# Kernel tuning notes

Measured on AMD Instinct MI355X. Metric: run time of the kernel, lower is better.

Reference implementation:

```python
import jax, jax.numpy as jnp
from jax import lax
import numpy as np

B, S, V, C, H, Z, NSTEP = 256, 128, 128, 16, 1024, 256, 128
VC = V * C


def _gru_cell(x, h, Wih, Whh, bih, bhh):
    # torch GRUCell: gates ordered r, z, n along rows of (3H, in)
    gi = x @ Wih.T + bih
    gh = h @ Whh.T + bhh
    ir, iz, inn = jnp.split(gi, 3, axis=-1)
    hr, hz, hn = jnp.split(gh, 3, axis=-1)
    r = jax.nn.sigmoid(ir + hr)
    zg = jax.nn.sigmoid(iz + hz)
    n = jnp.tanh(inn + r * hn)
    return (1.0 - zg) * n + zg * h


def setup_inputs() -> dict:
    key = jax.random.key(0)
    ks = jax.random.split(key, 32)
    sc = 0.05
    p = lambda k, shape: (jax.random.normal(k, shape, jnp.float32) * sc)
    inp = {
        "x": jax.random.normal(ks[0], (B, V, S), jnp.float32),
        "noise": jax.random.normal(ks[1], (B, Z), jnp.float32),
        "gruf_Wih": p(ks[2], (3 * H, V)), "gruf_Whh": p(ks[3], (3 * H, H)),
        "gruf_bih": p(ks[4], (3 * H,)), "gruf_bhh": p(ks[5], (3 * H,)),
        "grub_Wih": p(ks[6], (3 * H, V)), "grub_Whh": p(ks[7], (3 * H, H)),
        "grub_bih": p(ks[8], (3 * H,)), "grub_bhh": p(ks[9], (3 * H,)),
        "Wmu": p(ks[10], (Z, 2 * H)), "bmu": p(ks[11], (Z,)),
        "Wvar": p(ks[12], (Z, 2 * H)), "bvar": p(ks[13], (Z,)),
        "Winit": p(ks[14], (H, Z)), "binit": p(ks[15], (H,)),
        "c1_Wih": p(ks[16], (3 * H, Z + VC)), "c1_Whh": p(ks[17], (3 * H, H)),
        "c1_bih": p(ks[18], (3 * H,)), "c1_bhh": p(ks[19], (3 * H,)),
        "c2_Wih": p(ks[20], (3 * H, H)), "c2_Whh": p(ks[21], (3 * H, H)),
        "c2_bih": p(ks[22], (3 * H,)), "c2_bhh": p(ks[23], (3 * H,)),
        "Wout": p(ks[24], (VC, H)), "bout": p(ks[25], (VC,)),
    }
    return inp


def reference(x, noise, gruf_Wih, gruf_Whh, gruf_bih, gruf_bhh,
              grub_Wih, grub_Whh, grub_bih, grub_bhh,
              Wmu, bmu, Wvar, bvar, Winit, binit,
              c1_Wih, c1_Whh, c1_bih, c1_bhh,
              c2_Wih, c2_Whh, c2_bih, c2_bhh, Wout, bout):
    b = x.shape[0]
    xe = jnp.transpose(x, (0, 2, 1))           # (b, s, V)
    xt = jnp.swapaxes(xe, 0, 1)                # (s, b, V) time-major
    h0 = jnp.zeros((b, H), x.dtype)

    def step_f(h, xs):
        h2 = _gru_cell(xs, h, gruf_Wih, gruf_Whh, gruf_bih, gruf_bhh)
        return h2, None

    def step_b(h, xs):
        h2 = _gru_cell(xs, h, grub_Wih, grub_Whh, grub_bih, grub_bhh)
        return h2, None

    hf, _ = lax.scan(step_f, h0, xt)
    hb, _ = lax.scan(step_b, h0, xt[::-1])
    enc = jnp.concatenate([hf, hb], axis=-1)   # (b, 2H) = h_n transposed+flattened

    mu = enc @ Wmu.T + bmu
    var = jnp.exp(enc @ Wvar.T + bvar)         # Normal(mu, var): var is the scale
    z = mu + var * noise                       # rsample

    out0 = jnp.zeros((b, VC), x.dtype).at[:, -1].set(1.0)
    h1_0 = jnp.tanh(z @ Winit.T + binit)
    h2_0 = jnp.zeros((b, H), x.dtype)

    def dstep(carry, i):
        out, h1, h2 = carry
        inp = jnp.concatenate([out, z], axis=1)          # (b, VC + Z)
        h1n = _gru_cell(inp, h1, c1_Wih, c1_Whh, c1_bih, c1_bhh)
        h2_prev = jnp.where(i == 0, h1n, h2)             # hx[1] = hx[0] at step 0
        h2n = _gru_cell(h1n, h2_prev, c2_Wih, c2_Whh, c2_bih, c2_bhh)
        logits = h2n @ Wout.T + bout                     # (b, VC)
        ls = jax.nn.log_softmax(logits.reshape(b, C, V), axis=1).reshape(b, VC)
        # eval-mode _sampling: argmax -> one-hot (no gradient flows through it)
        out_n = jax.nn.one_hot(jnp.argmax(ls, axis=1), VC, dtype=ls.dtype)
        return (out_n, h1n, h2n), ls

    _, xs = lax.scan(dstep, (out0, h1_0, h2_0), jnp.arange(NSTEP))
    recon_seq = jnp.swapaxes(xs, 0, 1)                   # (b, n_step, VC)
    recon = jnp.transpose(recon_seq, (0, 2, 1)).reshape(b, C, V, NSTEP)
    return mu, var, z, recon
```

## Files before the change

kernel.cpp:

```cpp
#include <hip/hip_runtime.h>
#include <cstdint>
#include <cstddef>

typedef __attribute__((ext_vector_type(8))) short bf16x8;
typedef __attribute__((ext_vector_type(4))) float f32x4;
#define DEVI __device__ __forceinline__

constexpr int B = 256, S = 128, V = 128, C = 16, H = 1024, Z = 256, NSTEP = 128;
constexpr int VC = V * C, G3 = 3 * H;
constexpr size_t BVC = (size_t)B * VC;

typedef __attribute__((address_space(1))) const unsigned short* gas_p;
typedef __attribute__((address_space(3))) unsigned short* las_p;

DEVI unsigned short f2bf(float f){unsigned u=__float_as_uint(f);u+=0x7fffu+((u>>16)&1u);return (unsigned short)(u>>16);}
DEVI float sigm(float x){return 1.f/(1.f+expf(-x));}
DEVI f32x4 MFMA(bf16x8 a,bf16x8 b,f32x4 c){return __builtin_amdgcn_mfma_f32_16x16x32_bf16(a,b,c,0,0,0);}
DEVI void stage16(const unsigned short* g, unsigned short* l){__builtin_amdgcn_global_load_lds((gas_p)g,(las_p)l,16,0,0);}

DEVI unsigned long long ldc8(const void* p){return __hip_atomic_load((const unsigned long long*)p,__ATOMIC_RELAXED,__HIP_MEMORY_SCOPE_AGENT);}
DEVI void stc8(void* p, unsigned long long v){__hip_atomic_store((unsigned long long*)p,v,__ATOMIC_RELAXED,__HIP_MEMORY_SCOPE_AGENT);}
DEVI unsigned ldc4(const void* p){return __hip_atomic_load((const unsigned*)p,__ATOMIC_RELAXED,__HIP_MEMORY_SCOPE_AGENT);}
DEVI void stc4(void* p, unsigned v){__hip_atomic_store((unsigned*)p,v,__ATOMIC_RELAXED,__HIP_MEMORY_SCOPE_AGENT);}
DEVI unsigned long long pack4(float a,float b,float c,float d){
  return (unsigned long long)f2bf(a)|((unsigned long long)f2bf(b)<<16)|((unsigned long long)f2bf(c)<<32)|((unsigned long long)f2bf(d)<<48);
}
DEVI unsigned long long packf2(float a,float b){
  return (unsigned long long)__float_as_uint(a)|((unsigned long long)__float_as_uint(b)<<32);
}

DEVI void wv(int n){
  if(n==0)      asm volatile("s_waitcnt vmcnt(0)":::"memory");
  else if(n==2) asm volatile("s_waitcnt vmcnt(2)":::"memory");
  else if(n==3) asm volatile("s_waitcnt vmcnt(3)":::"memory");
  else if(n==4) asm volatile("s_waitcnt vmcnt(4)":::"memory");
  else if(n==6) asm volatile("s_waitcnt vmcnt(6)":::"memory");
}
DEVI void lg0(){asm volatile("s_waitcnt lgkmcnt(0)":::"memory");}
DEVI void cmb(){asm volatile("" ::: "memory");}

DEVI void waitflags(const unsigned* f,int base,int n,unsigned tgt){
  int lane=threadIdx.x&63;
  if (lane<n){
    const unsigned* a=&f[(size_t)(base+lane)<<4];
    while (ldc4(a)<tgt) __builtin_amdgcn_s_sleep(1);
  }
}
DEVI unsigned waitseq(const unsigned* f,int base,int n,unsigned tgt){
  int lane=threadIdx.x&63; unsigned v=tgt<<24;
  if (lane<n){
    const unsigned* a=&f[(size_t)(base+lane)<<4];
    v=ldc4(a);
    while ((v>>24)<tgt){__builtin_amdgcn_s_sleep(1); v=ldc4(a);}
  }
  return v;
}

__global__ void k_cvt(const float* __restrict__ src, unsigned short* __restrict__ dst, int n){
  for (int i=blockIdx.x*256+threadIdx.x;i<n;i+=gridDim.x*256) dst[i]=f2bf(src[i]);
}

__global__ void k_xt(const float* __restrict__ x, unsigned short* __restrict__ xtb){
  __shared__ float tile[32][33];
  int sb=blockIdx.x*32, rb=blockIdx.y*32, tx=threadIdx.x, ty=threadIdx.y;
  for (int i=ty;i<32;i+=8) tile[i][tx]=x[(size_t)(rb+i)*S+sb+tx];
  __syncthreads();
  for (int i=ty;i<32;i+=8) xtb[(size_t)(sb+i)*(B*V)+rb+tx]=f2bf(tile[tx][i]);
}

__global__ void k_wt(const float* __restrict__ w, float* __restrict__ wt){
  __shared__ float tile[32][33];
  int vb=blockIdx.x*32, nb=blockIdx.y*32, tx=threadIdx.x, ty=threadIdx.y;
  for (int i=ty;i<32;i+=8) tile[i][tx]=w[(size_t)(nb+i)*(VC+Z)+vb+tx];
  __syncthreads();
  for (int i=ty;i<32;i+=8) wt[(size_t)(vb+i)*G3+nb+tx]=tile[tx][i];
}

__global__ __launch_bounds__(256) void k_mu_var_z(const float* __restrict__ hf,const float* __restrict__ hb,
    const float* __restrict__ Wmu,const float* __restrict__ bmu,
    const float* __restrict__ Wvar,const float* __restrict__ bvar,
    const float* __restrict__ noise,
    float* __restrict__ omu,float* __restrict__ ovar,float* __restrict__ oz,float* __restrict__ zws){
  __shared__ float e[2*H];
  int b=blockIdx.x, t=threadIdx.x;
  for (int i=0;i<2*H/256;++i){int k=t+i*256; e[k]=(k<H)?hf[b*H+k]:hb[b*H+k-H];}
  __syncthreads();
  const float* wm=Wmu+(size_t)t*2*H; const float* wv2=Wvar+(size_t)t*2*H;
  float am=bmu[t], av=bvar[t];
  for (int k=0;k<2*H;++k){am+=e[k]*wm[k];av+=e[k]*wv2[k];}
  float vv=expf(av), zz=am+vv*noise[b*Z+t];
  omu[b*Z+t]=am; ovar[b*Z+t]=vv; oz[b*Z+t]=zz; zws[b*Z+t]=zz;
}

__global__ void k_zpart(const float* __restrict__ z,const float* __restrict__ c1Wih,
                        const float* __restrict__ bih,float* __restrict__ zpart){
  int idx=blockIdx.x*256+threadIdx.x;
  int b=idx/G3, n=idx%G3;
  const float* w=c1Wih+(size_t)n*(VC+Z)+VC;
  const float* zr=z+b*Z;
  float a=bih[n];
  for (int k=0;k<Z;++k) a+=zr[k]*w[k];
  zpart[idx]=a;
}

__global__ void k_h1init(const float* __restrict__ z,const float* __restrict__ Winit,
                         const float* __restrict__ binit,
                         float* __restrict__ h1f,unsigned short* __restrict__ h1b,unsigned* __restrict__ F4){
  int idx=blockIdx.x*256+threadIdx.x;
  int b=idx>>10, jj=idx&(H-1);
  const float* w=Winit+(size_t)jj*Z;
  const float* zr=z+b*Z;
  float a=binit[jj];
  for (int k=0;k<Z;++k) a+=zr[k]*w[k];
  float t=tanhf(a);
  h1f[idx]=t; h1b[idx]=f2bf(t);
  if (idx<128) F4[(size_t)idx<<4]=((unsigned)(VC-1)<<12)|(unsigned)(VC-1);
}

struct EncP {
  const unsigned short *xtb,*wihf,*whhf,*wihb,*whhb;
  const float *bihf,*bhhf,*bihb,*bhhb;
  unsigned short *hf0,*hf1,*hb0,*hb1;
  float *hf,*hb;
  unsigned* FE;
};

__global__ __launch_bounds__(512,1) void k_enc(EncP P){
  __shared__ unsigned short L[55296];
  const int tid=threadIdx.x, wave=tid>>6, lane=tid&63;
  const int l15=lane&15, l4=lane>>4;
  const int r8=lane>>2, pcl=lane&3;
  const int csw=(pcl-(r8>>1))&3;
  const int bid=blockIdx.x, jt=bid&7, mt=(bid>>3)&15, dir=bid>>7;
  const int g8=bid&~7;
  const unsigned short* wih=dir?P.wihb:P.wihf;
  const unsigned short* whh=dir?P.whhb:P.whhf;
  const float* bih=dir?P.bihb:P.bihf;
  const float* bhh=dir?P.bhhb:P.bhhf;
  unsigned short* hbuf[2]={dir?P.hb0:P.hf0, dir?P.hb1:P.hf1};
  const int m=mt*16+l15;
  const int j0=jt*128+wave*16+(l4<<2);
  const int WBe=18432;

  f32x4 cR,cZ,bNi,bNh;
  { f32x4 a=*(const f32x4*)&bih[j0],   b2=*(const f32x4*)&bhh[j0];   cR=a+b2; }
  { f32x4 a=*(const f32x4*)&bih[H+j0], b2=*(const f32x4*)&bhh[H+j0]; cZ=a+b2; }
  bNi=*(const f32x4*)&bih[2*H+j0]; bNh=*(const f32x4*)&bhh[2*H+j0];
  float hreg[4]={};

  auto W=[&](int kt,int buf){
    unsigned short* d=&L[WBe + wave*4608 + buf*1536];
    if (kt<32){
#pragma unroll
      for (int g=0;g<3;++g)
        stage16(whh + (size_t)((g<<10)+jt*128+wave*16+r8)*H + (kt<<5) + csw*8, d+(g<<9));
    } else {
      int kx=kt-32;
#pragma unroll
      for (int g=0;g<3;++g)
        stage16(wih + (size_t)((g<<10)+jt*128+wave*16+r8)*V + (kx<<5) + csw*8, d+(g<<9));
    }
    cmb();
  };

  for (int s=0;s<S;++s){
    waitflags(P.FE,g8,8,(unsigned)s);
    {
      const unsigned short* hs=hbuf[s&1] + (size_t)mt*16*H;
      unsigned long long q[8];
#pragma unroll
      for (int i=0;i<8;++i) q[i]=ldc8(hs + (i*512+tid)*4);
#pragma unroll
      for (int i=0;i<8;++i){
        int e=i*512+tid, row=e>>8, u=e&255, c=u>>1;
        int ph=(c&~7)|((c+(row>>1))&7);
        *(unsigned long long*)&L[row*1024 + ph*8 + (u&1)*4]=q[i];
      }
      const int xs=dir?(S-1-s):s;
      if (tid<256){
        int row=tid>>4, c=tid&15;
        uint4 v=*(const uint4*)&P.xtb[(size_t)xs*(B*V)+(size_t)(mt*16+row)*V+(c<<3)];
        int ph=(c&~7)|((c+(row>>1))&7);
        *(uint4*)&L[16384 + row*128 + ph*8]=v;
      }
    }
    __syncthreads();
    W(0,0); W(1,1); W(2,2);
    f32x4 aR={},aZ={},aNH={},aNX={};
    int buf=0;
    for (int kt=0;kt<36;++kt){
      if (kt<34) wv(6); else if (kt==34) wv(3); else wv(0);
      bf16x8 b;
      if (kt<32){
        int c=(kt<<2)+l4, ph=(c&~7)|((c+(l15>>1))&7);
        b=*(const bf16x8*)&L[l15*1024 + ph*8];
      } else {
        int c=((kt-32)<<2)+l4, ph=(c&~7)|((c+(l15>>1))&7);
        b=*(const bf16x8*)&L[16384 + l15*128 + ph*8];
      }
      int ab=WBe + wave*4608 + buf*1536 + l15*32 + (((l4+(l15>>1))&3)<<3);
      bf16x8 a0=*(const bf16x8*)&L[ab];
      bf16x8 a1=*(const bf16x8*)&L[ab+512];
      bf16x8 a2=*(const bf16x8*)&L[ab+1024];
      aR=MFMA(a0,b,aR); aZ=MFMA(a1,b,aZ);
      if (kt<32) aNH=MFMA(a2,b,aNH); else aNX=MFMA(a2,b,aNX);
      lg0();
      if (kt<33) W(kt+3,buf);
      buf=(buf==2)?0:buf+1;
    }
    float hv[4];
#pragma unroll
    for (int r=0;r<4;++r){
      float rg=sigm(aR[r]+cR[r]);
      float zg=sigm(aZ[r]+cZ[r]);
      float nn=tanhf(aNX[r]+bNi[r]+rg*(aNH[r]+bNh[r]));
      float hnew=(1.f-zg)*nn+zg*hreg[r];
      hreg[r]=hnew; hv[r]=hnew;
    }
    stc8(hbuf[(s+1)&1] + (size_t)m*H + j0, pack4(hv[0],hv[1],hv[2],hv[3]));
    wv(0); __syncthreads();
    if (tid==0) stc4(&P.FE[(size_t)bid<<4],(unsigned)(s+1));
  }
  float* hout=dir?P.hb:P.hf;
  f32x4 v; v[0]=hreg[0];v[1]=hreg[1];v[2]=hreg[2];v[3]=hreg[3];
  *(f32x4*)&hout[(size_t)m*H+j0]=v;
}

struct DecP {
  unsigned short *h1b0,*h1b1,*h2b0,*h2b1;
  const unsigned short *w1hh,*w2ih,*w2hh,*wout;
  const float *bhh1,*bih2,*bhh2,*bout;
  const float *zpart,*WT,*h1f;
  float *logits,*lsbuf,*recon;
  unsigned *F1,*F2,*F3,*F4;
};

__global__ __launch_bounds__(512,1) void k_dec(DecP P){
  __shared__ unsigned short L[69632];
  const int tid=threadIdx.x, wave=tid>>6, lane=tid&63;
  const int l15=lane&15, l4=lane>>4;
  const int r8=lane>>2, pcl=lane&3;
  const int csw=(pcl-(r8>>1))&3;
  const int bid=blockIdx.x, jb=bid&7, mt=bid>>3;
  const int g8=bid&~7;
  const int WB=32768;
  unsigned short* h1b[2]={P.h1b0,P.h1b1};
  unsigned short* h2b[2]={P.h2b0,P.h2b1};
  const int m=mt*16+l15;
  const int j0=jb*128+wave*16+(l4<<2);
  const int n0=jb*256+wave*32+(l4<<2);

  f32x4 zR4=*(const f32x4*)&P.zpart[(size_t)m*G3+j0];
  f32x4 zZ4=*(const f32x4*)&P.zpart[(size_t)m*G3+H+j0];
  f32x4 zN4=*(const f32x4*)&P.zpart[(size_t)m*G3+2*H+j0];
  f32x4 b1R=*(const f32x4*)&P.bhh1[j0], b1Z=*(const f32x4*)&P.bhh1[H+j0], b1N=*(const f32x4*)&P.bhh1[2*H+j0];
  f32x4 c2R,c2Z,biN2,bhN2;
  { f32x4 a=*(const f32x4*)&P.bih2[j0],   b2=*(const f32x4*)&P.bhh2[j0];   c2R=a+b2; }
  { f32x4 a=*(const f32x4*)&P.bih2[H+j0], b2=*(const f32x4*)&P.bhh2[H+j0]; c2Z=a+b2; }
  biN2=*(const f32x4*)&P.bih2[2*H+j0]; bhN2=*(const f32x4*)&P.bhh2[2*H+j0];
  f32x4 bo0=*(const f32x4*)&P.bout[n0];
  f32x4 bo1=*(const f32x4*)&P.bout[n0+16];
  f32x4 h1i=*(const f32x4*)&P.h1f[(size_t)m*H+j0];
  float h1reg[4]={h1i[0],h1i[1],h1i[2],h1i[3]};
  float h2reg[4]={};

  auto loadPanel=[&](const unsigned short* src,int base){
    const unsigned short* hs=src + (size_t)mt*16*H;
    unsigned long long q[8];
#pragma unroll
    for (int i=0;i<8;++i) q[i]=ldc8(hs + (i*512+tid)*4);
#pragma unroll
    for (int i=0;i<8;++i){
      int e=i*512+tid, row=e>>8, u=e&255, c=u>>1;
      int ph=(c&~7)|((c+(row>>1))&7);
      *(unsigned long long*)&L[base + row*1024 + ph*8 + (u&1)*4]=q[i];
    }
  };
  auto PFRAG=[&](int base,int kt)->bf16x8{
    int c=(kt<<2)+l4, ph=(c&~7)|((c+(l15>>1))&7);
    return *(const bf16x8*)&L[base + l15*1024 + ph*8];
  };
  auto W1=[&](int kt,int buf){
    unsigned short* d=&L[WB + wave*4608 + buf*1536];
#pragma unroll
    for (int g=0;g<3;++g)
      stage16(P.w1hh + (size_t)((g<<10)+jb*128+wave*16+r8)*H + (kt<<5) + csw*8, d+(g<<9));
    cmb();
  };
  auto W2=[&](int kt,int buf){
    unsigned short* d=&L[WB + wave*4608 + buf*1536];
    const unsigned short* src=(kt<32)?P.w2ih:P.w2hh;
    int ko=(kt<32)?(kt<<5):((kt-32)<<5);
#pragma unroll
    for (int g=0;g<3;++g)
      stage16(src + (size_t)((g<<10)+jb*128+wave*16+r8)*H + ko + csw*8, d+(g<<9));
    cmb();
  };
  auto W3=[&](int kt,int buf){
    unsigned short* d=&L[WB + wave*3072 + buf*1024];
#pragma unroll
    for (int nt=0;nt<2;++nt)
      stage16(P.wout + (size_t)(jb*256+wave*32+(nt<<4)+r8)*H + (kt<<5) + csw*8, d+(nt<<9));
    cmb();
  };

  loadPanel(h1b[0],0);

  for (int t=0;t<NSTEP;++t){
    const int cur=t&1, nxt=cur^1;
    {
      unsigned fv=waitseq(P.F4,g8,8,(unsigned)t);
      unsigned vv=__shfl(fv,(l15>>1));
      int idxm=(int)((vv>>(12*(l15&1)))&0xfffu);
      const float* wtr=P.WT+(size_t)idxm*G3;
      f32x4 wR=*(const f32x4*)&wtr[j0];
      f32x4 wZ=*(const f32x4*)&wtr[H+j0];
      f32x4 wN=*(const f32x4*)&wtr[2*H+j0];
      __syncthreads();
      W1(0,0); W1(1,1); W1(2,2);
      f32x4 aR={},aZ={},aN={};
      int buf=0;
      for (int kt=0;kt<32;++kt){
        if (kt<30) wv(6); else if (kt==30) wv(3); else wv(0);
        bf16x8 b=PFRAG(0,kt);
        int ab=WB + wave*4608 + buf*1536 + l15*32 + (((l4+(l15>>1))&3)<<3);
        bf16x8 a0=*(const bf16x8*)&L[ab];
        bf16x8 a1=*(const bf16x8*)&L[ab+512];
        bf16x8 a2=*(const bf16x8*)&L[ab+1024];
        aR=MFMA(a0,b,aR); aZ=MFMA(a1,b,aZ); aN=MFMA(a2,b,aN);
        lg0();
        if (kt<29) W1(kt+3,buf);
        buf=(buf==2)?0:buf+1;
      }
      float hv[4];
#pragma unroll
      for (int r=0;r<4;++r){
        float rg=sigm(zR4[r]+wR[r]+aR[r]+b1R[r]);
        float zg=sigm(zZ4[r]+wZ[r]+aZ[r]+b1Z[r]);
        float nn=tanhf(zN4[r]+wN[r]+rg*(aN[r]+b1N[r]));
        float hnew=(1.f-zg)*nn+zg*h1reg[r];
        h1reg[r]=hnew; hv[r]=hnew;
      }
      stc8(h1b[nxt]+(size_t)m*H+j0, pack4(hv[0],hv[1],hv[2],hv[3]));
      wv(0); __syncthreads();
      if (tid==0) stc4(&P.F1[(size_t)bid<<4],(unsigned)(t+1));
    }
    {
      waitflags(P.F1,g8,8,(unsigned)(t+1));
      loadPanel(h1b[nxt],0);
      loadPanel((t==0)?h1b[nxt]:h2b[cur],16384);
      __syncthreads();
      W2(0,0); W2(1,1); W2(2,2);
      f32x4 aR={},aZ={},aNI={},aNH={};
      int buf=0;
      for (int kt=0;kt<64;++kt){
        if (kt<62) wv(6); else if (kt==62) wv(3); else wv(0);
        bf16x8 b=(kt<32)?PFRAG(0,kt):PFRAG(16384,kt-32);
        int ab=WB + wave*4608 + buf*1536 + l15*32 + (((l4+(l15>>1))&3)<<3);
        bf16x8 a0=*(const bf16x8*)&L[ab];
        bf16x8 a1=*(const bf16x8*)&L[ab+512];
        bf16x8 a2=*(const bf16x8*)&L[ab+1024];
        aR=MFMA(a0,b,aR); aZ=MFMA(a1,b,aZ);
        if (kt<32) aNI=MFMA(a2,b,aNI); else aNH=MFMA(a2,b,aNH);
        lg0();
        if (kt<61) W2(kt+3,buf);
        buf=(buf==2)?0:buf+1;
      }
      float hv[4];
#pragma unroll
      for (int r=0;r<4;++r){
        float rg=sigm(aR[r]+c2R[r]);
        float zg=sigm(aZ[r]+c2Z[r]);
        float nn=tanhf(aNI[r]+biN2[r]+rg*(aNH[r]+bhN2[r]));
        float hp=(t==0)?h1reg[r]:h2reg[r];
        float hnew=(1.f-zg)*nn+zg*hp;
        h2reg[r]=hnew; hv[r]=hnew;
      }
      stc8(h2b[nxt]+(size_t)m*H+j0, pack4(hv[0],hv[1],hv[2],hv[3]));
      wv(0); __syncthreads();
      if (tid==0) stc4(&P.F2[(size_t)bid<<4],(unsigned)(t+1));
    }
    {
      waitflags(P.F2,g8,8,(unsigned)(t+1));
      loadPanel(h2b[nxt],0);
      __syncthreads();
      W3(0,0); W3(1,1); W3(2,2);
      f32x4 ac0={},ac1={};
      int buf=0;
      for (int kt=0;kt<32;++kt){
        if (kt<30) wv(4); else if (kt==30) wv(2); else wv(0);
        bf16x8 b=PFRAG(0,kt);
        int ab=WB + wave*3072 + buf*1024 + l15*32 + (((l4+(l15>>1))&3)<<3);
        bf16x8 a0=*(const bf16x8*)&L[ab];
        bf16x8 a1=*(const bf16x8*)&L[ab+512];
        ac0=MFMA(a0,b,ac0); ac1=MFMA(a1,b,ac1);
        lg0();
        if (kt<29) W3(kt+3,buf);
        buf=(buf==2)?0:buf+1;
      }
      stc8(&P.logits[(size_t)m*VC+n0],    packf2(ac0[0]+bo0[0],ac0[1]+bo0[1]));
      stc8(&P.logits[(size_t)m*VC+n0+2],  packf2(ac0[2]+bo0[2],ac0[3]+bo0[3]));
      stc8(&P.logits[(size_t)m*VC+n0+16], packf2(ac1[0]+bo1[0],ac1[1]+bo1[1]));
      stc8(&P.logits[(size_t)m*VC+n0+18], packf2(ac1[2]+bo1[2],ac1[3]+bo1[3]));
      wv(0); __syncthreads();
      if (tid==0) stc4(&P.F3[(size_t)bid<<4],(unsigned)(t+1));
    }
    {
      waitflags(P.F3,g8,8,(unsigned)(t+1));
      float* SM=(float*)&L[WB];
      const int row=tid>>8, t2=tid&255;
      const int b4=bid*2+row;
#pragma unroll
      for (int i=0;i<4;++i){
        unsigned long long q=ldc8(&P.logits[(size_t)b4*VC + t2*8 + i*2]);
        SM[row*2048+t2*8+i*2]  =__uint_as_float((unsigned)q);
        SM[row*2048+t2*8+i*2+1]=__uint_as_float((unsigned)(q>>32));
      }
      __syncthreads();
      if (t2<V){
        float mx=-1e30f;
        for (int c=0;c<C;++c) mx=fmaxf(mx,SM[row*2048+c*V+t2]);
        float su=0.f;
        for (int c=0;c<C;++c) su+=expf(SM[row*2048+c*V+t2]-mx);
        float lse=mx+logf(su);
        for (int c=0;c<C;++c) SM[row*2048+c*V+t2]-=lse;
      }
      __syncthreads();
      float bv=-1e30f; int bi=0;
#pragma unroll
      for (int i=0;i<8;++i){
        int n=t2*8+i; float v=SM[row*2048+n];
        if (v>bv){bv=v;bi=n;}
      }
      float* RV=SM+4096; int* RI=(int*)(SM+4608);
      RV[row*256+t2]=bv; RI[row*256+t2]=bi;
      __syncthreads();
      for (int s2=128;s2>0;s2>>=1){
        if (t2<s2){
          float v2=RV[row*256+t2+s2]; int i2=RI[row*256+t2+s2];
          if (v2>RV[row*256+t2]||(v2==RV[row*256+t2]&&i2<RI[row*256+t2])){RV[row*256+t2]=v2;RI[row*256+t2]=i2;}
        }
        __syncthreads();
      }
      float* dst=P.lsbuf+(size_t)(t&15)*BVC+(size_t)b4*VC;
#pragma unroll
      for (int i=0;i<4;++i)
        stc8(&dst[t2*8+i*2], packf2(SM[row*2048+t2*8+i*2],SM[row*2048+t2*8+i*2+1]));
      wv(0); __syncthreads();
      if (tid==0){
        unsigned i0=(unsigned)RI[0], i1=(unsigned)RI[256];
        stc4(&P.F4[(size_t)bid<<4], ((unsigned)(t+1)<<24)|(i1<<12)|i0);
      }
    }
    if ((t&15)==15){
      const int t0=t-15;
      const size_t e0=(size_t)bid*4096 + (size_t)tid*8;
#pragma unroll
      for (int pp=0;pp<4;++pp){
        float va[16],vb[16];
#pragma unroll
        for (int j2=0;j2<16;++j2){
          unsigned long long q=ldc8(&P.lsbuf[(size_t)j2*BVC + e0 + pp*2]);
          va[j2]=__uint_as_float((unsigned)q); vb[j2]=__uint_as_float((unsigned)(q>>32));
        }
        float* d0=&P.recon[(e0+pp*2)*NSTEP+t0];
        float* d1=&P.recon[(e0+pp*2+1)*NSTEP+t0];
#pragma unroll
        for (int k=0;k<16;++k){ d0[k]=va[k]; d1[k]=vb[k]; }
      }
    }
    loadPanel(h1b[nxt],0);
  }
}

extern "C" void kernel_launch(void* const* d_in, const int* in_sizes, int n_in,
                              void* d_out, int out_size, void* d_ws, size_t ws_size,
                              hipStream_t stream) {
  const float* x        = (const float*)d_in[0];
  const float* noise    = (const float*)d_in[1];
  const float* gruf_Wih = (const float*)d_in[2];
  const float* gruf_Whh = (const float*)d_in[3];
  const float* gruf_bih = (const float*)d_in[4];
  const float* gruf_bhh = (const float*)d_in[5];
  const float* grub_Wih = (const float*)d_in[6];
  const float* grub_Whh = (const float*)d_in[7];
  const float* grub_bih = (const float*)d_in[8];
  const float* grub_bhh = (const float*)d_in[9];
  const float* Wmu      = (const float*)d_in[10];
  const float* bmu      = (const float*)d_in[11];
  const float* Wvar     = (const float*)d_in[12];
  const float* bvar     = (const float*)d_in[13];
  const float* Winit    = (const float*)d_in[14];
  const float* binit    = (const float*)d_in[15];
  const float* c1_Wih   = (const float*)d_in[16];
  const float* c1_Whh   = (const float*)d_in[17];
  const float* c1_bih   = (const float*)d_in[18];
  const float* c1_bhh   = (const float*)d_in[19];
  const float* c2_Wih   = (const float*)d_in[20];
  const float* c2_Whh   = (const float*)d_in[21];
  const float* c2_bih   = (const float*)d_in[22];
  const float* c2_bhh   = (const float*)d_in[23];
  const float* Wout     = (const float*)d_in[24];
  const float* bout     = (const float*)d_in[25];

  float* omu = (float*)d_out;
  float* ovar = omu + B*Z;
  float* oz = ovar + B*Z;
  float* orecon = oz + B*Z;

  char* p = (char*)d_ws;
  auto carve = [&](size_t bytes){ char* r = p; p += (bytes+255)&~(size_t)255; return r; };
  unsigned short* wihf_b  = (unsigned short*)carve((size_t)G3*V*2);
  unsigned short* whhf_b  = (unsigned short*)carve((size_t)G3*H*2);
  unsigned short* wihb_b  = (unsigned short*)carve((size_t)G3*V*2);
  unsigned short* whhb_b  = (unsigned short*)carve((size_t)G3*H*2);
  unsigned short* wc1hh_b = (unsigned short*)carve((size_t)G3*H*2);
  unsigned short* wc2ih_b = (unsigned short*)carve((size_t)G3*H*2);
  unsigned short* wc2hh_b = (unsigned short*)carve((size_t)G3*H*2);
  unsigned short* wout_b  = (unsigned short*)carve((size_t)VC*H*2);
  unsigned short* xtb     = (unsigned short*)carve((size_t)S*B*V*2);
  unsigned short* hf0     = (unsigned short*)carve((size_t)B*H*2);
  unsigned short* hf1     = (unsigned short*)carve((size_t)B*H*2);
  unsigned short* hb0     = (unsigned short*)carve((size_t)B*H*2);
  unsigned short* hb1     = (unsigned short*)carve((size_t)B*H*2);
  unsigned short* h1b0    = (unsigned short*)carve((size_t)B*H*2);
  unsigned short* h1b1    = (unsigned short*)carve((size_t)B*H*2);
  unsigned short* h2b0    = (unsigned short*)carve((size_t)B*H*2);
  unsigned short* h2b1    = (unsigned short*)carve((size_t)B*H*2);
  float* WT     = (float*)carve((size_t)VC*G3*4);
  float* zpart  = (float*)carve((size_t)B*G3*4);
  float* hf     = (float*)carve((size_t)B*H*4);
  float* hb     = (float*)carve((size_t)B*H*4);
  float* h1f    = (float*)carve((size_t)B*H*4);
  float* zws    = (float*)carve((size_t)B*Z*4);
  float* logits = (float*)carve((size_t)B*VC*4);
  float* lsbuf  = (float*)carve((size_t)16*BVC*4);
  unsigned* FE  = (unsigned*)carve(16384);
  unsigned* F1  = (unsigned*)carve(8192);
  unsigned* F2  = (unsigned*)carve(8192);
  unsigned* F3  = (unsigned*)carve(8192);
  unsigned* F4  = (unsigned*)carve(8192);

  dim3 b256(256);
  auto cvt=[&](const float* s, unsigned short* d, int n){
    int nb=(n+255)/256; if (nb>2048) nb=2048;
    k_cvt<<<nb,b256,0,stream>>>(s,d,n);
  };
  cvt(gruf_Wih,wihf_b,G3*V);
  cvt(gruf_Whh,whhf_b,G3*H);
  cvt(grub_Wih,wihb_b,G3*V);
  cvt(grub_Whh,whhb_b,G3*H);
  cvt(c1_Whh,wc1hh_b,G3*H);
  cvt(c2_Wih,wc2ih_b,G3*H);
  cvt(c2_Whh,wc2hh_b,G3*H);
  cvt(Wout,wout_b,VC*H);
  k_xt<<<dim3(S/32,(B*V)/32),dim3(32,8),0,stream>>>(x,xtb);
  k_wt<<<dim3(VC/32,G3/32),dim3(32,8),0,stream>>>(c1_Wih,WT);
  hipMemsetAsync(hf0,0,(size_t)B*H*2,stream);
  hipMemsetAsync(hb0,0,(size_t)B*H*2,stream);
  hipMemsetAsync(FE,0,16384+4*8192,stream);

  EncP ep;
  ep.xtb=xtb; ep.wihf=wihf_b; ep.whhf=whhf_b; ep.wihb=wihb_b; ep.whhb=whhb_b;
  ep.bihf=gruf_bih; ep.bhhf=gruf_bhh; ep.bihb=grub_bih; ep.bhhb=grub_bhh;
  ep.hf0=hf0; ep.hf1=hf1; ep.hb0=hb0; ep.hb1=hb1;
  ep.hf=hf; ep.hb=hb; ep.FE=FE;
  k_enc<<<256,dim3(512),0,stream>>>(ep);

  k_mu_var_z<<<B,b256,0,stream>>>(hf,hb,Wmu,bmu,Wvar,bvar,noise,omu,ovar,oz,zws);
  k_zpart<<<B*G3/256,b256,0,stream>>>(zws,c1_Wih,c1_bih,zpart);
  k_h1init<<<B*H/256,b256,0,stream>>>(zws,Winit,binit,h1f,h1b0,F4);

  DecP dp;
  dp.h1b0=h1b0; dp.h1b1=h1b1; dp.h2b0=h2b0; dp.h2b1=h2b1;
  dp.w1hh=wc1hh_b; dp.w2ih=wc2ih_b; dp.w2hh=wc2hh_b; dp.wout=wout_b;
  dp.bhh1=c1_bhh; dp.bih2=c2_bih; dp.bhh2=c2_bhh; dp.bout=bout;
  dp.zpart=zpart; dp.WT=WT; dp.h1f=h1f;
  dp.logits=logits; dp.lsbuf=lsbuf; dp.recon=orecon;
  dp.F1=F1; dp.F2=F2; dp.F3=F3; dp.F4=F4;
  k_dec<<<128,dim3(512),0,stream>>>(dp);
}
```

Baseline: 9.206 ms.

## Retile persistent GRU kernels to 32-row batch tiles with direct global weight fragments

Encoder and decoder persistent kernels move from 16-row batch tiles with 128-column gate slices to 32-row batch tiles with 64-column slices, synchronised in groups of 16 blocks instead of 8. Weight fragments are now loaded directly from global memory into registers instead of being staged into LDS through global_load_lds triple buffers, and the hidden-state panel uses a padded row stride in place of the XOR swizzle. Per-block flag waits are spread across warps so each gathers its own 64-column slice once that producer is ready. In the decoder, the recurrent GEMMs that do not depend on the latest flag (h1 by Whh, h2 by Whh) are issued before waiting on the argmax and h1 flags, overlapping compute with synchronisation. This trades explicit LDS pipelining for reliance on L2/cache hits for weights, which could raise load latency.

```diff
diff --git a/kernel.cpp b/kernel.cpp
--- a/kernel.cpp
+++ b/kernel.cpp
@@ -9,14 +9,11 @@
 constexpr int B = 256, S = 128, V = 128, C = 16, H = 1024, Z = 256, NSTEP = 128;
 constexpr int VC = V * C, G3 = 3 * H;
 constexpr size_t BVC = (size_t)B * VC;
-
-typedef __attribute__((address_space(1))) const unsigned short* gas_p;
-typedef __attribute__((address_space(3))) unsigned short* las_p;
+constexpr int RS = 1032;
 
 DEVI unsigned short f2bf(float f){unsigned u=__float_as_uint(f);u+=0x7fffu+((u>>16)&1u);return (unsigned short)(u>>16);}
 DEVI float sigm(float x){return 1.f/(1.f+expf(-x));}
 DEVI f32x4 MFMA(bf16x8 a,bf16x8 b,f32x4 c){return __builtin_amdgcn_mfma_f32_16x16x32_bf16(a,b,c,0,0,0);}
-DEVI void stage16(const unsigned short* g, unsigned short* l){__builtin_amdgcn_global_load_lds((gas_p)g,(las_p)l,16,0,0);}
 
 DEVI unsigned long long ldc8(const void* p){return __hip_atomic_load((const unsigned long long*)p,__ATOMIC_RELAXED,__HIP_MEMORY_SCOPE_AGENT);}
 DEVI void stc8(void* p, unsigned long long v){__hip_atomic_store((unsigned long long*)p,v,__ATOMIC_RELAXED,__HIP_MEMORY_SCOPE_AGENT);}
@@ -28,24 +25,9 @@
 DEVI unsigned long long packf2(float a,float b){
   return (unsigned long long)__float_as_uint(a)|((unsigned long long)__float_as_uint(b)<<32);
 }
-
-DEVI void wv(int n){
-  if(n==0)      asm volatile("s_waitcnt vmcnt(0)":::"memory");
-  else if(n==2) asm volatile("s_waitcnt vmcnt(2)":::"memory");
-  else if(n==3) asm volatile("s_waitcnt vmcnt(3)":::"memory");
-  else if(n==4) asm volatile("s_waitcnt vmcnt(4)":::"memory");
-  else if(n==6) asm volatile("s_waitcnt vmcnt(6)":::"memory");
-}
-DEVI void lg0(){asm volatile("s_waitcnt lgkmcnt(0)":::"memory");}
 DEVI void cmb(){asm volatile("" ::: "memory");}
-
-DEVI void waitflags(const unsigned* f,int base,int n,unsigned tgt){
-  int lane=threadIdx.x&63;
-  if (lane<n){
-    const unsigned* a=&f[(size_t)(base+lane)<<4];
-    while (ldc4(a)<tgt) __builtin_amdgcn_s_sleep(1);
-  }
-}
+DEVI void drain(){asm volatile("s_waitcnt vmcnt(0) lgkmcnt(0)":::"memory");}
+
 DEVI unsigned waitseq(const unsigned* f,int base,int n,unsigned tgt){
   int lane=threadIdx.x&63; unsigned v=tgt<<24;
   if (lane<n){
@@ -53,6 +35,7 @@
     v=ldc4(a);
     while ((v>>24)<tgt){__builtin_amdgcn_s_sleep(1); v=ldc4(a);}
   }
+  cmb();
   return v;
 }
 
@@ -126,21 +109,21 @@
 };
 
 __global__ __launch_bounds__(512,1) void k_enc(EncP P){
-  __shared__ unsigned short L[55296];
+  __shared__ unsigned short L[37376];
+  const int XB=33024;
   const int tid=threadIdx.x, wave=tid>>6, lane=tid&63;
   const int l15=lane&15, l4=lane>>4;
-  const int r8=lane>>2, pcl=lane&3;
-  const int csw=(pcl-(r8>>1))&3;
-  const int bid=blockIdx.x, jt=bid&7, mt=(bid>>3)&15, dir=bid>>7;
-  const int g8=bid&~7;
-  const unsigned short* wih=dir?P.wihb:P.wihf;
-  const unsigned short* whh=dir?P.whhb:P.whhf;
+  const int bid=blockIdx.x, jt=bid&15, mgrp=(bid>>4)&7, dir=bid>>7;
+  const int g16=bid&~15;
+  const int jt4=wave>>1, mi=wave&1;
+  const int jrow=jt*64+jt4*16+l15;
+  const int j0=jt*64+jt4*16+(l4<<2);
+  const int m=mgrp*32+mi*16+l15;
+  const unsigned short* __restrict__ wih=dir?P.wihb:P.wihf;
+  const unsigned short* __restrict__ whh=dir?P.whhb:P.whhf;
   const float* bih=dir?P.bihb:P.bihf;
   const float* bhh=dir?P.bhhb:P.bhhf;
   unsigned short* hbuf[2]={dir?P.hb0:P.hf0, dir?P.hb1:P.hf1};
-  const int m=mt*16+l15;
-  const int j0=jt*128+wave*16+(l4<<2);
-  const int WBe=18432;
 
   f32x4 cR,cZ,bNi,bNh;
   { f32x4 a=*(const f32x4*)&bih[j0],   b2=*(const f32x4*)&bhh[j0];   cR=a+b2; }
@@ -148,65 +131,41 @@
   bNi=*(const f32x4*)&bih[2*H+j0]; bNh=*(const f32x4*)&bhh[2*H+j0];
   float hreg[4]={};
 
-  auto W=[&](int kt,int buf){
-    unsigned short* d=&L[WBe + wave*4608 + buf*1536];
-    if (kt<32){
-#pragma unroll
-      for (int g=0;g<3;++g)
-        stage16(whh + (size_t)((g<<10)+jt*128+wave*16+r8)*H + (kt<<5) + csw*8, d+(g<<9));
-    } else {
-      int kx=kt-32;
-#pragma unroll
-      for (int g=0;g<3;++g)
-        stage16(wih + (size_t)((g<<10)+jt*128+wave*16+r8)*V + (kx<<5) + csw*8, d+(g<<9));
-    }
-    cmb();
-  };
-
   for (int s=0;s<S;++s){
-    waitflags(P.FE,g8,8,(unsigned)s);
-    {
-      const unsigned short* hs=hbuf[s&1] + (size_t)mt*16*H;
-      unsigned long long q[8];
-#pragma unroll
-      for (int i=0;i<8;++i) q[i]=ldc8(hs + (i*512+tid)*4);
-#pragma unroll
-      for (int i=0;i<8;++i){
-        int e=i*512+tid, row=e>>8, u=e&255, c=u>>1;
-        int ph=(c&~7)|((c+(row>>1))&7);
-        *(unsigned long long*)&L[row*1024 + ph*8 + (u&1)*4]=q[i];
-      }
-      const int xs=dir?(S-1-s):s;
-      if (tid<256){
-        int row=tid>>4, c=tid&15;
-        uint4 v=*(const uint4*)&P.xtb[(size_t)xs*(B*V)+(size_t)(mt*16+row)*V+(c<<3)];
-        int ph=(c&~7)|((c+(row>>1))&7);
-        *(uint4*)&L[16384 + row*128 + ph*8]=v;
-      }
-    }
+    const int xs=dir?(S-1-s):s;
     __syncthreads();
-    W(0,0); W(1,1); W(2,2);
+    { int row=tid>>4, c=tid&15;
+      uint4 v=*(const uint4*)&P.xtb[(size_t)xs*(B*V)+(size_t)(mgrp*32+row)*V+(c<<3)];
+      *(uint4*)&L[XB + row*136 + (c<<3)]=v; }
+    { const int p=tid>>5, u=tid&31;
+      const unsigned* fa=&P.FE[(size_t)(g16+p)<<4];
+      while (ldc4(fa)<(unsigned)s) __builtin_amdgcn_s_sleep(1);
+      cmb();
+      const unsigned short* src=hbuf[s&1] + (size_t)(mgrp*32+u)*H + p*64;
+      unsigned long long q[16];
+#pragma unroll
+      for (int i=0;i<16;++i) q[i]=ldc8(src+i*4);
+      unsigned short* d=&L[u*RS + p*64];
+#pragma unroll
+      for (int i=0;i<16;++i) *(unsigned long long*)&d[i*4]=q[i];
+    }
+    __syncthreads();
     f32x4 aR={},aZ={},aNH={},aNX={};
-    int buf=0;
-    for (int kt=0;kt<36;++kt){
-      if (kt<34) wv(6); else if (kt==34) wv(3); else wv(0);
-      bf16x8 b;
-      if (kt<32){
-        int c=(kt<<2)+l4, ph=(c&~7)|((c+(l15>>1))&7);
-        b=*(const bf16x8*)&L[l15*1024 + ph*8];
-      } else {
-        int c=((kt-32)<<2)+l4, ph=(c&~7)|((c+(l15>>1))&7);
-        b=*(const bf16x8*)&L[16384 + l15*128 + ph*8];
-      }
-      int ab=WBe + wave*4608 + buf*1536 + l15*32 + (((l4+(l15>>1))&3)<<3);
-      bf16x8 a0=*(const bf16x8*)&L[ab];
-      bf16x8 a1=*(const bf16x8*)&L[ab+512];
-      bf16x8 a2=*(const bf16x8*)&L[ab+1024];
-      aR=MFMA(a0,b,aR); aZ=MFMA(a1,b,aZ);
-      if (kt<32) aNH=MFMA(a2,b,aNH); else aNX=MFMA(a2,b,aNX);
-      lg0();
-      if (kt<33) W(kt+3,buf);
-      buf=(buf==2)?0:buf+1;
+#pragma unroll 4
+    for (int kk=0;kk<32;++kk){
+      bf16x8 b=*(const bf16x8*)&L[(mi*16+l15)*RS + kk*32 + l4*8];
+      bf16x8 a0=*(const bf16x8*)&whh[(size_t)(jrow      )*H + kk*32 + l4*8];
+      bf16x8 a1=*(const bf16x8*)&whh[(size_t)(H   +jrow )*H + kk*32 + l4*8];
+      bf16x8 a2=*(const bf16x8*)&whh[(size_t)(2*H +jrow )*H + kk*32 + l4*8];
+      aR=MFMA(a0,b,aR); aZ=MFMA(a1,b,aZ); aNH=MFMA(a2,b,aNH);
+    }
+#pragma unroll
+    for (int kk=0;kk<4;++kk){
+      bf16x8 b=*(const bf16x8*)&L[XB + (mi*16+l15)*136 + kk*32 + l4*8];
+      bf16x8 a0=*(const bf16x8*)&wih[(size_t)(jrow      )*V + kk*32 + l4*8];
+      bf16x8 a1=*(const bf16x8*)&wih[(size_t)(H   +jrow )*V + kk*32 + l4*8];
+      bf16x8 a2=*(const bf16x8*)&wih[(size_t)(2*H +jrow )*V + kk*32 + l4*8];
+      aR=MFMA(a0,b,aR); aZ=MFMA(a1,b,aZ); aNX=MFMA(a2,b,aNX);
     }
     float hv[4];
 #pragma unroll
@@ -218,7 +177,7 @@
       hreg[r]=hnew; hv[r]=hnew;
     }
     stc8(hbuf[(s+1)&1] + (size_t)m*H + j0, pack4(hv[0],hv[1],hv[2],hv[3]));
-    wv(0); __syncthreads();
+    drain(); __syncthreads();
     if (tid==0) stc4(&P.FE[(size_t)bid<<4],(unsigned)(s+1));
   }
   float* hout=dir?P.hb:P.hf;
@@ -236,19 +195,20 @@
 };
 
 __global__ __launch_bounds__(512,1) void k_dec(DecP P){
-  __shared__ unsigned short L[69632];
+  __shared__ unsigned short L[76288];
+  const int PB=33024, SMB=66048;
   const int tid=threadIdx.x, wave=tid>>6, lane=tid&63;
   const int l15=lane&15, l4=lane>>4;
-  const int r8=lane>>2, pcl=lane&3;
-  const int csw=(pcl-(r8>>1))&3;
-  const int bid=blockIdx.x, jb=bid&7, mt=bid>>3;
-  const int g8=bid&~7;
-  const int WB=32768;
+  const int bid=blockIdx.x, jb=bid&15, mgrp=bid>>4;
+  const int g16=bid&~15;
+  const int jt4=wave>>1, mi=wave&1;
+  const int jrow=jb*64+jt4*16+l15;
+  const int j0=jb*64+jt4*16+(l4<<2);
+  const int m=mgrp*32+mi*16+l15;
+  const int nrow0=jb*128+jt4*32+l15;
+  const int n0=jb*128+jt4*32+(l4<<2);
   unsigned short* h1b[2]={P.h1b0,P.h1b1};
   unsigned short* h2b[2]={P.h2b0,P.h2b1};
-  const int m=mt*16+l15;
-  const int j0=jb*128+wave*16+(l4<<2);
-  const int n0=jb*256+wave*32+(l4<<2);
 
   f32x4 zR4=*(const f32x4*)&P.zpart[(size_t)m*G3+j0];
   f32x4 zZ4=*(const f32x4*)&P.zpart[(size_t)m*G3+H+j0];
@@ -264,74 +224,54 @@
   float h1reg[4]={h1i[0],h1i[1],h1i[2],h1i[3]};
   float h2reg[4]={};
 
-  auto loadPanel=[&](const unsigned short* src,int base){
-    const unsigned short* hs=src + (size_t)mt*16*H;
-    unsigned long long q[8];
-#pragma unroll
-    for (int i=0;i<8;++i) q[i]=ldc8(hs + (i*512+tid)*4);
-#pragma unroll
-    for (int i=0;i<8;++i){
-      int e=i*512+tid, row=e>>8, u=e&255, c=u>>1;
-      int ph=(c&~7)|((c+(row>>1))&7);
-      *(unsigned long long*)&L[base + row*1024 + ph*8 + (u&1)*4]=q[i];
-    }
+  auto gather=[&](int base, const unsigned short* src, unsigned* F, unsigned tgt){
+    const int p=tid>>5, u=tid&31;
+    const unsigned* fa=&F[(size_t)(g16+p)<<4];
+    while (ldc4(fa)<tgt) __builtin_amdgcn_s_sleep(1);
+    cmb();
+    const unsigned short* s=src + (size_t)(mgrp*32+u)*H + p*64;
+    unsigned long long q[16];
+#pragma unroll
+    for (int i=0;i<16;++i) q[i]=ldc8(s+i*4);
+    unsigned short* d=&L[base + u*RS + p*64];
+#pragma unroll
+    for (int i=0;i<16;++i) *(unsigned long long*)&d[i*4]=q[i];
   };
-  auto PFRAG=[&](int base,int kt)->bf16x8{
-    int c=(kt<<2)+l4, ph=(c&~7)|((c+(l15>>1))&7);
-    return *(const bf16x8*)&L[base + l15*1024 + ph*8];
+  auto PF=[&](int base,int kk)->bf16x8{
+    return *(const bf16x8*)&L[base + (mi*16+l15)*RS + kk*32 + l4*8];
   };
-  auto W1=[&](int kt,int buf){
-    unsigned short* d=&L[WB + wave*4608 + buf*1536];
-#pragma unroll
-    for (int g=0;g<3;++g)
-      stage16(P.w1hh + (size_t)((g<<10)+jb*128+wave*16+r8)*H + (kt<<5) + csw*8, d+(g<<9));
-    cmb();
-  };
-  auto W2=[&](int kt,int buf){
-    unsigned short* d=&L[WB + wave*4608 + buf*1536];
-    const unsigned short* src=(kt<32)?P.w2ih:P.w2hh;
-    int ko=(kt<32)?(kt<<5):((kt-32)<<5);
-#pragma unroll
-    for (int g=0;g<3;++g)
-      stage16(src + (size_t)((g<<10)+jb*128+wave*16+r8)*H + ko + csw*8, d+(g<<9));
-    cmb();
-  };
-  auto W3=[&](int kt,int buf){
-    unsigned short* d=&L[WB + wave*3072 + buf*1024];
-#pragma unroll
-    for (int nt=0;nt<2;++nt)
-      stage16(P.wout + (size_t)(jb*256+wave*32+(nt<<4)+r8)*H + (kt<<5) + csw*8, d+(nt<<9));
-    cmb();
-  };
-
-  loadPanel(h1b[0],0);
+
+  { const int p=tid>>5, u=tid&31;
+    const unsigned short* s=P.h1b0 + (size_t)(mgrp*32+u)*H + p*64;
+    unsigned long long q[16];
+#pragma unroll
+    for (int i=0;i<16;++i) q[i]=ldc8(s+i*4);
+    unsigned short* d=&L[u*RS + p*64];
+#pragma unroll
+    for (int i=0;i<16;++i) *(unsigned long long*)&d[i*4]=q[i];
+  }
+  __syncthreads();
 
   for (int t=0;t<NSTEP;++t){
     const int cur=t&1, nxt=cur^1;
     {
-      unsigned fv=waitseq(P.F4,g8,8,(unsigned)t);
-      unsigned vv=__shfl(fv,(l15>>1));
-      int idxm=(int)((vv>>(12*(l15&1)))&0xfffu);
+      f32x4 aR={},aZ={},aN={};
+#pragma unroll 4
+      for (int kk=0;kk<32;++kk){
+        bf16x8 b=PF(0,kk);
+        bf16x8 a0=*(const bf16x8*)&P.w1hh[(size_t)(jrow      )*H + kk*32 + l4*8];
+        bf16x8 a1=*(const bf16x8*)&P.w1hh[(size_t)(H   +jrow )*H + kk*32 + l4*8];
+        bf16x8 a2=*(const bf16x8*)&P.w1hh[(size_t)(2*H +jrow )*H + kk*32 + l4*8];
+        aR=MFMA(a0,b,aR); aZ=MFMA(a1,b,aZ); aN=MFMA(a2,b,aN);
+      }
+      unsigned fv=waitseq(P.F4,g16,16,(unsigned)t);
+      int rr=mi*16+l15;
+      unsigned vv=__shfl(fv,rr>>1);
+      int idxm=(int)((vv>>(12*(rr&1)))&0xfffu);
       const float* wtr=P.WT+(size_t)idxm*G3;
       f32x4 wR=*(const f32x4*)&wtr[j0];
       f32x4 wZ=*(const f32x4*)&wtr[H+j0];
       f32x4 wN=*(const f32x4*)&wtr[2*H+j0];
-      __syncthreads();
-      W1(0,0); W1(1,1); W1(2,2);
-      f32x4 aR={},aZ={},aN={};
-      int buf=0;
-      for (int kt=0;kt<32;++kt){
-        if (kt<30) wv(6); else if (kt==30) wv(3); else wv(0);
-        bf16x8 b=PFRAG(0,kt);
-        int ab=WB + wave*4608 + buf*1536 + l15*32 + (((l4+(l15>>1))&3)<<3);
-        bf16x8 a0=*(const bf16x8*)&L[ab];
-        bf16x8 a1=*(const bf16x8*)&L[ab+512];
-        bf16x8 a2=*(const bf16x8*)&L[ab+1024];
-        aR=MFMA(a0,b,aR); aZ=MFMA(a1,b,aZ); aN=MFMA(a2,b,aN);
-        lg0();
-        if (kt<29) W1(kt+3,buf);
-        buf=(buf==2)?0:buf+1;
-      }
       float hv[4];
 #pragma unroll
       for (int r=0;r<4;++r){
@@ -342,29 +282,36 @@
         h1reg[r]=hnew; hv[r]=hnew;
       }
       stc8(h1b[nxt]+(size_t)m*H+j0, pack4(hv[0],hv[1],hv[2],hv[3]));
-      wv(0); __syncthreads();
+      drain(); __syncthreads();
       if (tid==0) stc4(&P.F1[(size_t)bid<<4],(unsigned)(t+1));
     }
     {
-      waitflags(P.F1,g8,8,(unsigned)(t+1));
-      loadPanel(h1b[nxt],0);
-      loadPanel((t==0)?h1b[nxt]:h2b[cur],16384);
+      f32x4 aR={},aZ={},aNI={},aNH={};
+      if (t>0){
+#pragma unroll 4
+        for (int kk=0;kk<32;++kk){
+          bf16x8 b=PF(PB,kk);
+          bf16x8 a0=*(const bf16x8*)&P.w2hh[(size_t)(jrow      )*H + kk*32 + l4*8];
+          bf16x8 a1=*(const bf16x8*)&P.w2hh[(size_t)(H   +jrow )*H + kk*32 + l4*8];
+          bf16x8 a2=*(const bf16x8*)&P.w2hh[(size_t)(2*H +jrow )*H + kk*32 + l4*8];
+          aR=MFMA(a0,b,aR); aZ=MFMA(a1,b,aZ); aNH=MFMA(a2,b,aNH);
+        }
+      }
+      gather(0, h1b[nxt], P.F1, (unsigned)(t+1));
       __syncthreads();
-      W2(0,0); W2(1,1); W2(2,2);
-      f32x4 aR={},aZ={},aNI={},aNH={};
-      int buf=0;
-      for (int kt=0;kt<64;++kt){
-        if (kt<62) wv(6); else if (kt==62) wv(3); else wv(0);
-        bf16x8 b=(kt<32)?PFRAG(0,kt):PFRAG(16384,kt-32);
-        int ab=WB + wave*4608 + buf*1536 + l15*32 + (((l4+(l15>>1))&3)<<3);
-        bf16x8 a0=*(const bf16x8*)&L[ab];
-        bf16x8 a1=*(const bf16x8*)&L[ab+512];
-        bf16x8 a2=*(const bf16x8*)&L[ab+1024];
-        aR=MFMA(a0,b,aR); aZ=MFMA(a1,b,aZ);
-        if (kt<32) aNI=MFMA(a2,b,aNI); else aNH=MFMA(a2,b,aNH);
-        lg0();
-        if (kt<61) W2(kt+3,buf);
-        buf=(buf==2)?0:buf+1;
+#pragma unroll 2
+      for (int kk=0;kk<32;++kk){
+        bf16x8 b=PF(0,kk);
+        bf16x8 a0=*(const bf16x8*)&P.w2ih[(size_t)(jrow      )*H + kk*32 + l4*8];
+        bf16x8 a1=*(const bf16x8*)&P.w2ih[(size_t)(H   +jrow )*H + kk*32 + l4*8];
+        bf16x8 a2=*(const bf16x8*)&P.w2ih[(size_t)(2*H +jrow )*H + kk*32 + l4*8];
+        aR=MFMA(a0,b,aR); aZ=MFMA(a1,b,aZ); aNI=MFMA(a2,b,aNI);
+        if (t==0){
+          bf16x8 c0=*(const bf16x8*)&P.w2hh[(size_t)(jrow      )*H + kk*32 + l4*8];
+          bf16x8 c1=*(const bf16x8*)&P.w2hh[(size_t)(H   +jrow )*H + kk*32 + l4*8];
+          bf16x8 c2=*(const bf16x8*)&P.w2hh[(size_t)(2*H +jrow )*H + kk*32 + l4*8];
+          aR=MFMA(c0,b,aR); aZ=MFMA(c1,b,aZ); aNH=MFMA(c2,b,aNH);
+        }
       }
       float hv[4];
 #pragma unroll
@@ -377,46 +324,44 @@
         h2reg[r]=hnew; hv[r]=hnew;
       }
       stc8(h2b[nxt]+(size_t)m*H+j0, pack4(hv[0],hv[1],hv[2],hv[3]));
-      wv(0); __syncthreads();
+      drain(); __syncthreads();
       if (tid==0) stc4(&P.F2[(size_t)bid<<4],(unsigned)(t+1));
     }
     {
-      waitflags(P.F2,g8,8,(unsigned)(t+1));
-      loadPanel(h2b[nxt],0);
+      gather(PB, h2b[nxt], P.F2, (unsigned)(t+1));
       __syncthreads();
-      W3(0,0); W3(1,1); W3(2,2);
       f32x4 ac0={},ac1={};
-      int buf=0;
-      for (int kt=0;kt<32;++kt){
-        if (kt<30) wv(4); else if (kt==30) wv(2); else wv(0);
-        bf16x8 b=PFRAG(0,kt);
-        int ab=WB + wave*3072 + buf*1024 + l15*32 + (((l4+(l15>>1))&3)<<3);
-        bf16x8 a0=*(const bf16x8*)&L[ab];
-        bf16x8 a1=*(const bf16x8*)&L[ab+512];
+#pragma unroll 4
+      for (int kk=0;kk<32;++kk){
+        bf16x8 b=PF(PB,kk);
+        bf16x8 a0=*(const bf16x8*)&P.wout[(size_t)(nrow0   )*H + kk*32 + l4*8];
+        bf16x8 a1=*(const bf16x8*)&P.wout[(size_t)(nrow0+16)*H + kk*32 + l4*8];
         ac0=MFMA(a0,b,ac0); ac1=MFMA(a1,b,ac1);
-        lg0();
-        if (kt<29) W3(kt+3,buf);
-        buf=(buf==2)?0:buf+1;
       }
       stc8(&P.logits[(size_t)m*VC+n0],    packf2(ac0[0]+bo0[0],ac0[1]+bo0[1]));
       stc8(&P.logits[(size_t)m*VC+n0+2],  packf2(ac0[2]+bo0[2],ac0[3]+bo0[3]));
       stc8(&P.logits[(size_t)m*VC+n0+16], packf2(ac1[0]+bo1[0],ac1[1]+bo1[1]));
       stc8(&P.logits[(size_t)m*VC+n0+18], packf2(ac1[2]+bo1[2],ac1[3]+bo1[3]));
-      wv(0); __syncthreads();
+      drain(); __syncthreads();
       if (tid==0) stc4(&P.F3[(size_t)bid<<4],(unsigned)(t+1));
     }
     {
-      waitflags(P.F3,g8,8,(unsigned)(t+1));
-      float* SM=(float*)&L[WB];
+      float* SM=(float*)&L[SMB];
+      { const int p=tid>>5, u=tid&31;
+        const unsigned* fa=&P.F3[(size_t)(g16+p)<<4];
+        while (ldc4(fa)<(unsigned)(t+1)) __builtin_amdgcn_s_sleep(1);
+        cmb();
+        const int row=u>>4, c0=(u&15)*8;
+        const float* s=&P.logits[(size_t)(2*bid+row)*VC + p*128 + c0];
+#pragma unroll
+        for (int i=0;i<4;++i){
+          unsigned long long q=ldc8(s+i*2);
+          SM[row*2048 + p*128 + c0 + i*2]   = __uint_as_float((unsigned)q);
+          SM[row*2048 + p*128 + c0 + i*2+1] = __uint_as_float((unsigned)(q>>32));
+        }
+      }
+      __syncthreads();
       const int row=tid>>8, t2=tid&255;
-      const int b4=bid*2+row;
-#pragma unroll
-      for (int i=0;i<4;++i){
-        unsigned long long q=ldc8(&P.logits[(size_t)b4*VC + t2*8 + i*2]);
-        SM[row*2048+t2*8+i*2]  =__uint_as_float((unsigned)q);
-        SM[row*2048+t2*8+i*2+1]=__uint_as_float((unsigned)(q>>32));
-      }
-      __syncthreads();
       if (t2<V){
         float mx=-1e30f;
         for (int c=0;c<C;++c) mx=fmaxf(mx,SM[row*2048+c*V+t2]);
@@ -442,11 +387,11 @@
         }
         __syncthreads();
       }
-      float* dst=P.lsbuf+(size_t)(t&15)*BVC+(size_t)b4*VC;
+      float* dst=P.lsbuf+(size_t)(t&15)*BVC+(size_t)(2*bid+row)*VC;
 #pragma unroll
       for (int i=0;i<4;++i)
         stc8(&dst[t2*8+i*2], packf2(SM[row*2048+t2*8+i*2],SM[row*2048+t2*8+i*2+1]));
-      wv(0); __syncthreads();
+      drain(); __syncthreads();
       if (tid==0){
         unsigned i0=(unsigned)RI[0], i1=(unsigned)RI[256];
         stc4(&P.F4[(size_t)bid<<4], ((unsigned)(t+1)<<24)|(i1<<12)|i0);
@@ -469,7 +414,6 @@
         for (int k=0;k<16;++k){ d0[k]=va[k]; d1[k]=vb[k]; }
       }
     }
-    loadPanel(h1b[nxt],0);
   }
 }
 
```

After: 17.62 ms. +91.4%, slower.
